# Kernel tuning notes

Measured on AMD Instinct MI355X. Metric: run time of the kernel, lower is better.

The kernel has to match this reference:

```python
import jax, jax.numpy as jnp
import numpy as np

B, S, D, H = 2, 2048, 1024, 16
HD = D // H  # head dim = 64


def setup_inputs() -> dict:
    key = jax.random.key(0)
    ks = jax.random.split(key, 5)
    scale = 0.02
    x = jax.random.normal(ks[0], (B, S, D), dtype=jnp.float32)
    Wqkv = jax.random.normal(ks[1], (D, 3 * D), dtype=jnp.float32) * scale
    bqkv = jnp.zeros((3 * D,), dtype=jnp.float32)
    Wproj = jax.random.normal(ks[2], (D, D), dtype=jnp.float32) * scale
    bproj = jnp.zeros((D,), dtype=jnp.float32)
    return {"x": x, "Wqkv": Wqkv, "bqkv": bqkv, "Wproj": Wproj, "bproj": bproj}


def reference(x, Wqkv, bqkv, Wproj, bproj):
    # fused QKV projection
    qkv = x @ Wqkv + bqkv                      # [B, S, 3D]
    q, k, v = jnp.split(qkv, 3, axis=-1)       # each [B, S, D]
    # split heads -> [B, H, S, HD]
    def heads(t):
        return t.reshape(B, S, H, HD).transpose(0, 2, 1, 3)
    q, k, v = heads(q), heads(k), heads(v)
    # scaled dot-product attention with causal mask (GPT-2 style)
    scores = jnp.einsum('bhqd,bhkd->bhqk', q, k) / jnp.sqrt(jnp.float32(HD))
    causal = jnp.tril(jnp.ones((S, S), dtype=bool))
    scores = jnp.where(causal, scores, jnp.finfo(scores.dtype).min)
    attn = jax.nn.softmax(scores, axis=-1)      # [B, H, S, S]
    out = jnp.einsum('bhqk,bhkd->bhqd', attn, v)  # [B, H, S, HD]
    out = out.transpose(0, 2, 1, 3).reshape(B, S, D)
    return out @ Wproj + bproj
```

## Files before the change

### kernel.cpp

```cpp
#include <hip/hip_runtime.h>
#include <hip/hip_bf16.h>


typedef __attribute__((ext_vector_type(8))) short short8;
typedef __attribute__((ext_vector_type(4))) float float4v;

#define S_LEN 2048
#define NHEAD 16
#define HDIM  64
#define DMODEL 1024

__device__ __forceinline__ unsigned short f2bf(float f) {
    union { float f; unsigned u; } v; v.f = f;
    unsigned r = v.u + 0x7FFF + ((v.u >> 16) & 1);
    return (unsigned short)(r >> 16);
}

__device__ __forceinline__ unsigned fbits_rn(float f) {
    union { float f; unsigned u; } v; v.f = f;
    return v.u + 0x8000u;
}

__device__ __forceinline__ void async16(const void* g, const void* l) {
    __builtin_amdgcn_global_load_lds(
        (const __attribute__((address_space(1))) unsigned int*)g,
        (__attribute__((address_space(3))) unsigned int*)l, 16, 0, 0);
}

__global__ void f32_to_bf16_v4(const float4* __restrict__ in,
                               ushort4* __restrict__ out, int n4) {
    int i = blockIdx.x * blockDim.x + threadIdx.x;
    if (i < n4) {
        float4 v = in[i];
        ushort4 o;
        o.x = f2bf(v.x); o.y = f2bf(v.y); o.z = f2bf(v.z); o.w = f2bf(v.w);
        out[i] = o;
    }
}

__global__ __launch_bounds__(256) void w_transpose_bf16(
    const float* __restrict__ Wqkv, const float* __restrict__ Wproj,
    unsigned short* __restrict__ outQ, unsigned short* __restrict__ outP) {
    __shared__ float t[64][65];
    const float* in; unsigned short* out; int N, bxl;
    if (blockIdx.x < 48) { in = Wqkv;  out = outQ; N = 3072; bxl = blockIdx.x; }
    else                 { in = Wproj; out = outP; N = 1024; bxl = blockIdx.x - 48; }
    const int K = 1024;
    const int kb = blockIdx.y * 64, nb = bxl * 64;
    const int tid = threadIdx.x;
    const int r0 = tid >> 4, c0 = (tid & 15) * 4;
#pragma unroll
    for (int g = 0; g < 4; g++) {
        float4 v = *(const float4*)(in + (size_t)(kb + g * 16 + r0) * N + nb + c0);
        t[g * 16 + r0][c0 + 0] = v.x; t[g * 16 + r0][c0 + 1] = v.y;
        t[g * 16 + r0][c0 + 2] = v.z; t[g * 16 + r0][c0 + 3] = v.w;
    }
    __syncthreads();
#pragma unroll
    for (int g = 0; g < 4; g++) {
        int n = g * 16 + r0;
        ushort4 o;
        o.x = f2bf(t[c0 + 0][n]); o.y = f2bf(t[c0 + 1][n]);
        o.z = f2bf(t[c0 + 2][n]); o.w = f2bf(t[c0 + 3][n]);
        *(ushort4*)(out + (size_t)(nb + n) * K + kb + c0) = o;
    }
}

__global__ __launch_bounds__(256) void v_pack(
    const unsigned short* __restrict__ V, unsigned short* __restrict__ Vp) {
    __shared__ unsigned short t[64 * 68];
    const int bh = blockIdx.y;
    const int c0 = blockIdx.x;
    const int s0 = c0 * 64;
    const int tid = threadIdx.x;
    const int r = tid >> 2, c4 = tid & 3;
    const size_t base = (size_t)bh * S_LEN * HDIM;
    union { uint4 v[2]; unsigned short u[16]; } d;
    const unsigned short* src = V + base + (size_t)(s0 + r) * HDIM + c4 * 16;
    d.v[0] = *(const uint4*)(src);
    d.v[1] = *(const uint4*)(src + 8);
#pragma unroll
    for (int j = 0; j < 16; j++) t[r * 68 + c4 * 16 + j] = d.u[j];
    __syncthreads();
    unsigned short* outb = Vp + ((size_t)(bh * 32 + c0)) * 4096;
#pragma unroll
    for (int pi = 0; pi < 2; pi++) {
        const int p = tid * 2 + pi;
        const int lane = p & 63, kk = (p >> 6) & 1, nt = p >> 7;
        const int q = lane >> 4, l = lane & 15;
        union { ushort4 v[2]; unsigned short u[8]; } w;
#pragma unroll
        for (int j = 0; j < 8; j++) {
            const int key = (kk * 2 + (j >> 2)) * 16 + q * 4 + (j & 3);
            w.u[j] = t[key * 68 + nt * 16 + l];
        }
        unsigned short* po = outb + ((nt * 2 + kk) * 64 + lane) * 8;
        *(ushort4*)(po) = w.v[0];
        *(ushort4*)(po + 4) = w.v[1];
    }
}

#define QSCALE 0.18033688f

__global__ __launch_bounds__(256) void gemm_qkv_kernel(
    const unsigned short* __restrict__ A,
    const unsigned short* __restrict__ Bt,
    const float* __restrict__ bias,
    unsigned short* __restrict__ out_q,
    unsigned short* __restrict__ out_kp,
    unsigned short* __restrict__ out_v,
    int M, int N, int K)
{
    __shared__ unsigned short smem[128 * 132];
    unsigned short* As = smem;
    unsigned short* Bs = smem + 8192;

    const int tid  = threadIdx.x;
    const int lane = tid & 63;
    const int wave = tid >> 6;
    const int quad = lane >> 4;
    const int l16  = lane & 15;

    const int m0 = blockIdx.y * 128;
    const int n0 = blockIdx.x * 128;
    const int wm = (wave >> 1) * 64;
    const int wn = (wave & 1) * 64;

    float4v acc[4][4];
#pragma unroll
    for (int i = 0; i < 4; i++)
#pragma unroll
        for (int j = 0; j < 4; j++) acc[i][j] = (float4v){0.f, 0.f, 0.f, 0.f};

    const int srow = lane >> 2;
    const int scol = (lane & 3) * 8;

    for (int k0 = 0; k0 < K; k0 += 64) {
        __syncthreads();
#pragma unroll
        for (int kk = 0; kk < 2; kk++)
#pragma unroll
            for (int it = 0; it < 2; it++) {
                const int rg = it * 64 + wave * 16;
                async16(A  + (size_t)(m0 + rg + srow) * K + k0 + kk * 32 + scol,
                        (const char*)(As + kk * 4096) + rg * 64);
                async16(Bt + (size_t)(n0 + rg + srow) * K + k0 + kk * 32 + scol,
                        (const char*)(Bs + kk * 4096) + rg * 64);
            }
        __syncthreads();

#pragma unroll
        for (int kk = 0; kk < 2; kk++) {
            short8 af[4], bf[4];
#pragma unroll
            for (int mt = 0; mt < 4; mt++)
                af[mt] = *(const short8*)(As + kk * 4096
                                          + (wm + mt * 16 + l16) * 32 + quad * 8);
#pragma unroll
            for (int nt = 0; nt < 4; nt++)
                bf[nt] = *(const short8*)(Bs + kk * 4096
                                          + (wn + nt * 16 + l16) * 32 + quad * 8);
#pragma unroll
            for (int mt = 0; mt < 4; mt++)
#pragma unroll
                for (int nt = 0; nt < 4; nt++)
                    acc[mt][nt] = __builtin_amdgcn_mfma_f32_16x16x32_bf16(
                        af[mt], bf[nt], acc[mt][nt], 0, 0, 0);
        }
    }

    __syncthreads();
#pragma unroll
    for (int nt = 0; nt < 4; nt++) {
        const int col = n0 + wn + nt * 16 + l16;
        const float sc = ((col >> 10) == 0) ? QSCALE : 1.0f;
        const float bia = bias[col] * sc;
        const int cold = (wn + nt * 16 + l16) >> 1;
#pragma unroll
        for (int mt = 0; mt < 4; mt++)
#pragma unroll
            for (int r = 0; r < 4; r++) {
                unsigned fb = fbits_rn(acc[mt][nt][r] * sc + bia);
                unsigned fbp = (unsigned)__shfl_xor((int)fb, 1, 64);
                unsigned pd = (l16 & 1)
                    ? __builtin_amdgcn_perm(fb, fbp, 0x07060302)
                    : __builtin_amdgcn_perm(fbp, fb, 0x07060302);
                const int rowl = wm + mt * 16 + quad * 4 + r;
                *((unsigned*)smem + rowl * 66 + cold) = pd;
            }
    }
    __syncthreads();

#pragma unroll
    for (int ps = 0; ps < 8; ps++) {
        const int row = ps * 16 + (tid >> 4);
        const int pc  = tid & 15;
        const int col0 = pc * 8;
        const int cb = n0 + (col0 >> 6) * 64;
        const int part = cb >> 10;
        const int hh = (cb & 1023) >> 6;
        const int gr = m0 + row;
        const int b = gr >> 11, s = gr & 2047;
        const size_t bhI = (size_t)(b * NHEAD + hh);
        const unsigned short* pl = smem + row * 132 + col0;
        uint2 a = *(const uint2*)(pl);
        uint2 bb = *(const uint2*)(pl + 4);
        uint4 w; w.x = a.x; w.y = a.y; w.z = bb.x; w.w = bb.y;
        unsigned short* po;
        if (part == 1) {
            const int hd = col0 & 63;
            const int h = hd >> 5, q = (hd >> 3) & 3;
            po = out_kp + ((((bhI * 32 + (s >> 6)) * 4 + ((s >> 4) & 3)) * 2 + h)
                           * 64 + q * 16 + (s & 15)) * 8;
        } else {
            unsigned short* dst = (part == 0) ? out_q : out_v;
            po = dst + (bhI * S_LEN + s) * HDIM + (col0 & 63);
        }
        *(uint4*)po = w;
    }
}

__global__ __launch_bounds__(256) void gemm_proj_kernel(
    const unsigned short* __restrict__ A,
    const unsigned short* __restrict__ Bt,
    const float* __restrict__ bias,
    float* __restrict__ out_f,
    int M, int N, int K)
{
    __shared__ unsigned short smem[12288];
    unsigned short* As = smem;
    unsigned short* Bs = smem + 4096;

    const int tid  = threadIdx.x;
    const int lane = tid & 63;
    const int wave = tid >> 6;
    const int quad = lane >> 4;
    const int l16  = lane & 15;

    const int m0 = blockIdx.y * 64;
    const int n0 = blockIdx.x * 128;
    const int wm = (wave >> 1) * 32;
    const int wn = (wave & 1) * 64;

    float4v acc[2][4];
#pragma unroll
    for (int i = 0; i < 2; i++)
#pragma unroll
        for (int j = 0; j < 4; j++) acc[i][j] = (float4v){0.f, 0.f, 0.f, 0.f};

    const int srow = lane >> 2;
    const int scol = (lane & 3) * 8;

    for (int k0 = 0; k0 < K; k0 += 64) {
        __syncthreads();
#pragma unroll
        for (int kk = 0; kk < 2; kk++) {
            async16(A + (size_t)(m0 + wave * 16 + srow) * K + k0 + kk * 32 + scol,
                    (const char*)(As + kk * 2048) + wave * 1024);
#pragma unroll
            for (int it = 0; it < 2; it++) {
                const int rg = it * 64 + wave * 16;
                async16(Bt + (size_t)(n0 + rg + srow) * K + k0 + kk * 32 + scol,
                        (const char*)(Bs + kk * 4096) + rg * 64);
            }
        }
        __syncthreads();

#pragma unroll
        for (int kk = 0; kk < 2; kk++) {
            short8 af[2], bf[4];
#pragma unroll
            for (int mt = 0; mt < 2; mt++)
                af[mt] = *(const short8*)(As + kk * 2048
                                          + (wm + mt * 16 + l16) * 32 + quad * 8);
#pragma unroll
            for (int nt = 0; nt < 4; nt++)
                bf[nt] = *(const short8*)(Bs + kk * 4096
                                          + (wn + nt * 16 + l16) * 32 + quad * 8);
#pragma unroll
            for (int mt = 0; mt < 2; mt++)
#pragma unroll
                for (int nt = 0; nt < 4; nt++)
                    acc[mt][nt] = __builtin_amdgcn_mfma_f32_16x16x32_bf16(
                        af[mt], bf[nt], acc[mt][nt], 0, 0, 0);
        }
    }

#pragma unroll
    for (int nt = 0; nt < 4; nt++) {
        const int col = n0 + wn + nt * 16 + l16;
        const float bia = bias[col];
#pragma unroll
        for (int mt = 0; mt < 2; mt++) {
            const int rowb = m0 + wm + mt * 16 + quad * 4;
#pragma unroll
            for (int r = 0; r < 4; r++)
                out_f[(size_t)(rowb + r) * N + col] = acc[mt][nt][r] + bia;
        }
    }
}

__global__ __launch_bounds__(256) void attn6_kernel(
    const unsigned short* __restrict__ Q,
    const unsigned short* __restrict__ Kp,
    const unsigned short* __restrict__ Vp,
    unsigned short* __restrict__ ctx)
{
    __shared__ unsigned short lds[2][8192];

    const int tid  = threadIdx.x;
    const int lane = tid & 63;
    const int wave = tid >> 6;
    const int quad = lane >> 4;
    const int l16  = lane & 15;

    const int bx = blockIdx.x;
    const int bh = bx & 31;
    const int qb = 31 - (bx >> 5);
    const int q0 = qb * 64 + wave * 16;
    const int nch = qb + 1;

    const size_t baseQ = (size_t)bh * S_LEN * HDIM;
    const unsigned short* kb_ = Kp + (size_t)bh * 32 * 4096;
    const unsigned short* vb_ = Vp + (size_t)bh * 32 * 4096;

    short8 qf[2];
#pragma unroll
    for (int h = 0; h < 2; h++)
        qf[h] = *(const short8*)(Q + baseQ + (size_t)(q0 + l16) * HDIM
                                 + h * 32 + quad * 8);

    float4v o[4];
#pragma unroll
    for (int nt = 0; nt < 4; nt++) o[nt] = (float4v){0.f, 0.f, 0.f, 0.f};
    float lsa[4] = {0.f, 0.f, 0.f, 0.f};

    {
        unsigned short* sb = &lds[0][0];
        async16(kb_ + tid * 8,        sb + wave * 512);
        async16(kb_ + 2048 + tid * 8, sb + 2048 + wave * 512);
        async16(vb_ + tid * 8,        sb + 4096 + wave * 512);
        async16(vb_ + 2048 + tid * 8, sb + 6144 + wave * 512);
    }

    for (int c = 0; c < nch; c++) {
        __syncthreads();
        const unsigned short* lb = &lds[c & 1][0];

        short8 kf[4][2];
#pragma unroll
        for (int kt = 0; kt < 4; kt++)
#pragma unroll
            for (int h = 0; h < 2; h++)
                kf[kt][h] = *(const short8*)(lb + ((kt * 2 + h) * 64 + lane) * 8);

        if (c + 1 < nch) {
            const unsigned short* kc = kb_ + (size_t)(c + 1) * 4096;
            const unsigned short* vc = vb_ + (size_t)(c + 1) * 4096;
            unsigned short* sb = &lds[(c + 1) & 1][0];
            async16(kc + tid * 8,        sb + wave * 512);
            async16(kc + 2048 + tid * 8, sb + 2048 + wave * 512);
            async16(vc + tid * 8,        sb + 4096 + wave * 512);
            async16(vc + 2048 + tid * 8, sb + 6144 + wave * 512);
        }

        float4v st[4];
#pragma unroll
        for (int kt = 0; kt < 4; kt++) {
            st[kt] = __builtin_amdgcn_mfma_f32_16x16x32_bf16(
                kf[kt][0], qf[0], (float4v){0.f, 0.f, 0.f, 0.f}, 0, 0, 0);
            st[kt] = __builtin_amdgcn_mfma_f32_16x16x32_bf16(
                kf[kt][1], qf[1], st[kt], 0, 0, 0);
        }

        short8 vf[4][2];
#pragma unroll
        for (int nt = 0; nt < 4; nt++)
#pragma unroll
            for (int kk = 0; kk < 2; kk++)
                vf[nt][kk] = *(const short8*)(lb + 4096
                                              + ((nt * 2 + kk) * 64 + lane) * 8);

        const bool lastc = (c == nch - 1);
        const int kb0 = c * 64;
        const int qpos = q0 + l16;
        float p[4][4];
#pragma unroll
        for (int kt = 0; kt < 4; kt++)
#pragma unroll
            for (int r = 0; r < 4; r++) {
                float x = st[kt][r];
                if (lastc) {
                    int kpos = kb0 + kt * 16 + quad * 4 + r;
                    x = (kpos <= qpos) ? x : -1e30f;
                }
                p[kt][r] = __builtin_amdgcn_exp2f(x);
                lsa[kt] += p[kt][r];
            }

        unsigned pk[4][2];
#pragma unroll
        for (int kt = 0; kt < 4; kt++)
#pragma unroll
            for (int j = 0; j < 2; j++)
                pk[kt][j] = __builtin_amdgcn_perm(
                    fbits_rn(p[kt][2 * j + 1]), fbits_rn(p[kt][2 * j]),
                    0x07060302);
        union { unsigned u[4]; short8 s; } pf[2];
#pragma unroll
        for (int kk = 0; kk < 2; kk++)
#pragma unroll
            for (int pp = 0; pp < 4; pp++)
                pf[kk].u[pp] = pk[kk * 2 + (pp >> 1)][pp & 1];

#pragma unroll
        for (int nt = 0; nt < 4; nt++) {
            o[nt] = __builtin_amdgcn_mfma_f32_16x16x32_bf16(
                pf[0].s, vf[nt][0], o[nt], 0, 0, 0);
            o[nt] = __builtin_amdgcn_mfma_f32_16x16x32_bf16(
                pf[1].s, vf[nt][1], o[nt], 0, 0, 0);
        }
    }

    float l = (lsa[0] + lsa[1]) + (lsa[2] + lsa[3]);
    l += __shfl_xor(l, 16, 64);
    l += __shfl_xor(l, 32, 64);
    const float linv = 1.f / l;
    float lr[4];
#pragma unroll
    for (int r = 0; r < 4; r++) lr[r] = __shfl(linv, quad * 4 + r, 64);

    const int b = bh >> 4, h = bh & 15;
#pragma unroll
    for (int r = 0; r < 4; r++) {
        const int s = q0 + quad * 4 + r;
        const size_t off = ((size_t)(b * S_LEN + s)) * DMODEL + h * HDIM;
#pragma unroll
        for (int nt = 0; nt < 4; nt++)
            ctx[off + nt * 16 + l16] = f2bf(o[nt][r] * lr[r]);
    }
}

extern "C" void kernel_launch(void* const* d_in, const int* in_sizes, int n_in,
                              void* d_out, int out_size, void* d_ws, size_t ws_size,
                              hipStream_t stream) {
    const float* x     = (const float*)d_in[0];
    const float* Wqkv  = (const float*)d_in[1];
    const float* bqkv  = (const float*)d_in[2];
    const float* Wproj = (const float*)d_in[3];
    const float* bproj = (const float*)d_in[4];
    float* out = (float*)d_out;

    const int M  = 2 * S_LEN;
    const int N1 = 3 * DMODEL;
    const int K  = DMODEL;

    unsigned short* x_bf    = (unsigned short*)d_ws;
    unsigned short* wqkv_t  = x_bf   + (size_t)M * K;
    unsigned short* wproj_t = wqkv_t + (size_t)K * N1;
    unsigned short* q_bf    = wproj_t + (size_t)K * DMODEL;
    unsigned short* kp_bf   = q_bf   + (size_t)M * DMODEL;
    unsigned short* v_bf    = kp_bf  + (size_t)M * DMODEL;
    unsigned short* ctx_bf  = v_bf   + (size_t)M * DMODEL;
    unsigned short* vp_bf   = x_bf;

    {
        int n4 = (M * K) / 4;
        f32_to_bf16_v4<<<n4 / 256, 256, 0, stream>>>((const float4*)x,
                                                     (ushort4*)x_bf, n4);
    }
    {
        dim3 g(64, 16);
        w_transpose_bf16<<<g, 256, 0, stream>>>(Wqkv, Wproj, wqkv_t, wproj_t);
    }

    dim3 g1(N1 / 128, M / 128);
    gemm_qkv_kernel<<<g1, 256, 0, stream>>>(x_bf, wqkv_t, bqkv,
                                            q_bf, kp_bf, v_bf, M, N1, K);

    {
        dim3 g(S_LEN / 64, 2 * NHEAD);
        v_pack<<<g, 256, 0, stream>>>(v_bf, vp_bf);
    }

    attn6_kernel<<<1024, 256, 0, stream>>>(q_bf, kp_bf, vp_bf, ctx_bf);

    dim3 g3(DMODEL / 128, M / 64);
    gemm_proj_kernel<<<g3, 256, 0, stream>>>(ctx_bf, wproj_t, bproj, out,
                                             M, DMODEL, K);
}
```

Baseline: 172.3 us.

## Double query tile per attention block to reuse K/V loads across 128 queries

Each attention block now covers 128 query rows (32 per wave, two 16-row MFMA tiles) instead of 64, so each K/V chunk staged in LDS serves twice as many queries and the grid halves to 512 blocks. Block order is interleaved so heavy and light causal blocks are mixed, and waves skip chunks that lie entirely beyond their causal range. Masking is applied per tile only where needed. In exchange each thread holds more registers for two sets of accumulators, and waves within a block have uneven work near the diagonal.

Result: slower. 184.1 us (+6.9%).

```diff
diff --git a/kernel.cpp b/kernel.cpp
--- a/kernel.cpp
+++ b/kernel.cpp
@@ -300,7 +300,7 @@
     }
 }
 
-__global__ __launch_bounds__(256) void attn6_kernel(
+__global__ __launch_bounds__(256, 2) void attn7_kernel(
     const unsigned short* __restrict__ Q,
     const unsigned short* __restrict__ Kp,
     const unsigned short* __restrict__ Vp,
@@ -316,24 +316,34 @@
 
     const int bx = blockIdx.x;
     const int bh = bx & 31;
-    const int qb = 31 - (bx >> 5);
-    const int q0 = qb * 64 + wave * 16;
-    const int nch = qb + 1;
+    const int g  = bx >> 5;
+    const int qb = (g < 8) ? (15 - g) : (g - 8);
+    const int q0w = qb * 128 + wave * 32;
+    const int nch = 2 * qb + 2;
 
     const size_t baseQ = (size_t)bh * S_LEN * HDIM;
     const unsigned short* kb_ = Kp + (size_t)bh * 32 * 4096;
     const unsigned short* vb_ = Vp + (size_t)bh * 32 * 4096;
 
-    short8 qf[2];
-#pragma unroll
-    for (int h = 0; h < 2; h++)
-        qf[h] = *(const short8*)(Q + baseQ + (size_t)(q0 + l16) * HDIM
-                                 + h * 32 + quad * 8);
-
-    float4v o[4];
-#pragma unroll
-    for (int nt = 0; nt < 4; nt++) o[nt] = (float4v){0.f, 0.f, 0.f, 0.f};
-    float lsa[4] = {0.f, 0.f, 0.f, 0.f};
+    short8 qf[2][2];
+#pragma unroll
+    for (int qt = 0; qt < 2; qt++)
+#pragma unroll
+        for (int h = 0; h < 2; h++)
+            qf[qt][h] = *(const short8*)(Q + baseQ
+                                         + (size_t)(q0w + qt * 16 + l16) * HDIM
+                                         + h * 32 + quad * 8);
+
+    float4v o[2][4];
+#pragma unroll
+    for (int qt = 0; qt < 2; qt++)
+#pragma unroll
+        for (int nt = 0; nt < 4; nt++) o[qt][nt] = (float4v){0.f, 0.f, 0.f, 0.f};
+    float lsa[2][4];
+#pragma unroll
+    for (int qt = 0; qt < 2; qt++)
+#pragma unroll
+        for (int kt = 0; kt < 4; kt++) lsa[qt][kt] = 0.f;
 
     {
         unsigned short* sb = &lds[0][0];
@@ -346,13 +356,18 @@
     for (int c = 0; c < nch; c++) {
         __syncthreads();
         const unsigned short* lb = &lds[c & 1][0];
+        const int kb0 = c * 64;
+        const bool wactive = (kb0 <= q0w + 31);
 
         short8 kf[4][2];
-#pragma unroll
-        for (int kt = 0; kt < 4; kt++)
-#pragma unroll
-            for (int h = 0; h < 2; h++)
-                kf[kt][h] = *(const short8*)(lb + ((kt * 2 + h) * 64 + lane) * 8);
+        if (wactive) {
+#pragma unroll
+            for (int kt = 0; kt < 4; kt++)
+#pragma unroll
+                for (int h = 0; h < 2; h++)
+                    kf[kt][h] = *(const short8*)(lb
+                                                 + ((kt * 2 + h) * 64 + lane) * 8);
+        }
 
         if (c + 1 < nch) {
             const unsigned short* kc = kb_ + (size_t)(c + 1) * 4096;
@@ -364,80 +379,90 @@
             async16(vc + 2048 + tid * 8, sb + 6144 + wave * 512);
         }
 
-        float4v st[4];
-#pragma unroll
-        for (int kt = 0; kt < 4; kt++) {
-            st[kt] = __builtin_amdgcn_mfma_f32_16x16x32_bf16(
-                kf[kt][0], qf[0], (float4v){0.f, 0.f, 0.f, 0.f}, 0, 0, 0);
-            st[kt] = __builtin_amdgcn_mfma_f32_16x16x32_bf16(
-                kf[kt][1], qf[1], st[kt], 0, 0, 0);
-        }
-
-        short8 vf[4][2];
-#pragma unroll
-        for (int nt = 0; nt < 4; nt++)
-#pragma unroll
-            for (int kk = 0; kk < 2; kk++)
-                vf[nt][kk] = *(const short8*)(lb + 4096
-                                              + ((nt * 2 + kk) * 64 + lane) * 8);
-
-        const bool lastc = (c == nch - 1);
-        const int kb0 = c * 64;
-        const int qpos = q0 + l16;
-        float p[4][4];
-#pragma unroll
-        for (int kt = 0; kt < 4; kt++)
-#pragma unroll
-            for (int r = 0; r < 4; r++) {
-                float x = st[kt][r];
-                if (lastc) {
-                    int kpos = kb0 + kt * 16 + quad * 4 + r;
-                    x = (kpos <= qpos) ? x : -1e30f;
+        if (wactive) {
+            float4v st[2][4];
+#pragma unroll
+            for (int qt = 0; qt < 2; qt++)
+#pragma unroll
+                for (int kt = 0; kt < 4; kt++) {
+                    st[qt][kt] = __builtin_amdgcn_mfma_f32_16x16x32_bf16(
+                        kf[kt][0], qf[qt][0], (float4v){0.f, 0.f, 0.f, 0.f},
+                        0, 0, 0);
+                    st[qt][kt] = __builtin_amdgcn_mfma_f32_16x16x32_bf16(
+                        kf[kt][1], qf[qt][1], st[qt][kt], 0, 0, 0);
                 }
-                p[kt][r] = __builtin_amdgcn_exp2f(x);
-                lsa[kt] += p[kt][r];
+
+            short8 vf[4][2];
+#pragma unroll
+            for (int nt = 0; nt < 4; nt++)
+#pragma unroll
+                for (int kk = 0; kk < 2; kk++)
+                    vf[nt][kk] = *(const short8*)(lb + 4096
+                                                  + ((nt * 2 + kk) * 64 + lane) * 8);
+
+#pragma unroll
+            for (int qt = 0; qt < 2; qt++) {
+                const int q0t = q0w + qt * 16;
+                const bool needmask = (kb0 + 63 > q0t);
+                const int qpos = q0t + l16;
+                float p[4][4];
+#pragma unroll
+                for (int kt = 0; kt < 4; kt++)
+#pragma unroll
+                    for (int r = 0; r < 4; r++) {
+                        float x = st[qt][kt][r];
+                        if (needmask) {
+                            int kpos = kb0 + kt * 16 + quad * 4 + r;
+                            x = (kpos <= qpos) ? x : -1e30f;
+                        }
+                        p[kt][r] = __builtin_amdgcn_exp2f(x);
+                        lsa[qt][kt] += p[kt][r];
+                    }
+
+                unsigned pk[4][2];
+#pragma unroll
+                for (int kt = 0; kt < 4; kt++)
+#pragma unroll
+                    for (int j = 0; j < 2; j++)
+                        pk[kt][j] = __builtin_amdgcn_perm(
+                            fbits_rn(p[kt][2 * j + 1]), fbits_rn(p[kt][2 * j]),
+                            0x07060302);
+                union { unsigned u[4]; short8 s; } pf[2];
+#pragma unroll
+                for (int kk = 0; kk < 2; kk++)
+#pragma unroll
+                    for (int pp = 0; pp < 4; pp++)
+                        pf[kk].u[pp] = pk[kk * 2 + (pp >> 1)][pp & 1];
+
+#pragma unroll
+                for (int nt = 0; nt < 4; nt++) {
+                    o[qt][nt] = __builtin_amdgcn_mfma_f32_16x16x32_bf16(
+                        pf[0].s, vf[nt][0], o[qt][nt], 0, 0, 0);
+                    o[qt][nt] = __builtin_amdgcn_mfma_f32_16x16x32_bf16(
+                        pf[1].s, vf[nt][1], o[qt][nt], 0, 0, 0);
+                }
             }
-
-        unsigned pk[4][2];
-#pragma unroll
-        for (int kt = 0; kt < 4; kt++)
-#pragma unroll
-            for (int j = 0; j < 2; j++)
-                pk[kt][j] = __builtin_amdgcn_perm(
-                    fbits_rn(p[kt][2 * j + 1]), fbits_rn(p[kt][2 * j]),
-                    0x07060302);
-        union { unsigned u[4]; short8 s; } pf[2];
-#pragma unroll
-        for (int kk = 0; kk < 2; kk++)
-#pragma unroll
-            for (int pp = 0; pp < 4; pp++)
-                pf[kk].u[pp] = pk[kk * 2 + (pp >> 1)][pp & 1];
-
-#pragma unroll
-        for (int nt = 0; nt < 4; nt++) {
-            o[nt] = __builtin_amdgcn_mfma_f32_16x16x32_bf16(
-                pf[0].s, vf[nt][0], o[nt], 0, 0, 0);
-            o[nt] = __builtin_amdgcn_mfma_f32_16x16x32_bf16(
-                pf[1].s, vf[nt][1], o[nt], 0, 0, 0);
-        }
-    }
-
-    float l = (lsa[0] + lsa[1]) + (lsa[2] + lsa[3]);
-    l += __shfl_xor(l, 16, 64);
-    l += __shfl_xor(l, 32, 64);
-    const float linv = 1.f / l;
-    float lr[4];
-#pragma unroll
-    for (int r = 0; r < 4; r++) lr[r] = __shfl(linv, quad * 4 + r, 64);
+        }
+    }
 
     const int b = bh >> 4, h = bh & 15;
 #pragma unroll
-    for (int r = 0; r < 4; r++) {
-        const int s = q0 + quad * 4 + r;
-        const size_t off = ((size_t)(b * S_LEN + s)) * DMODEL + h * HDIM;
-#pragma unroll
-        for (int nt = 0; nt < 4; nt++)
-            ctx[off + nt * 16 + l16] = f2bf(o[nt][r] * lr[r]);
+    for (int qt = 0; qt < 2; qt++) {
+        float l = (lsa[qt][0] + lsa[qt][1]) + (lsa[qt][2] + lsa[qt][3]);
+        l += __shfl_xor(l, 16, 64);
+        l += __shfl_xor(l, 32, 64);
+        const float linv = 1.f / l;
+        float lr[4];
+#pragma unroll
+        for (int r = 0; r < 4; r++) lr[r] = __shfl(linv, quad * 4 + r, 64);
+#pragma unroll
+        for (int r = 0; r < 4; r++) {
+            const int s = q0w + qt * 16 + quad * 4 + r;
+            const size_t off = ((size_t)(b * S_LEN + s)) * DMODEL + h * HDIM;
+#pragma unroll
+            for (int nt = 0; nt < 4; nt++)
+                ctx[off + nt * 16 + l16] = f2bf(o[qt][nt][r] * lr[r]);
+        }
     }
 }
 
@@ -483,7 +508,7 @@
         v_pack<<<g, 256, 0, stream>>>(v_bf, vp_bf);
     }
 
-    attn6_kernel<<<1024, 256, 0, stream>>>(q_bf, kp_bf, vp_bf, ctx_bf);
+    attn7_kernel<<<512, 256, 0, stream>>>(q_bf, kp_bf, vp_bf, ctx_bf);
 
     dim3 g3(DMODEL / 128, M / 64);
     gemm_proj_kernel<<<g3, 256, 0, stream>>>(ctx_bf, wproj_t, bproj, out,
```

## Split attention KV range in two halves and combine partials

Applied to the files above, without the earlier changes.

Each query block's causal KV chunk range is split across two workgroups (split-K style). Each writes unnormalized fp32 partial outputs and row sums to workspace, and a new combine kernel sums them, normalizes and writes bf16 context. This is meant to cut the load imbalance and tail of long causal rows, since 1024 blocks became 2048 with shorter work. In exchange it adds an extra kernel launch and about 33 MB of fp32 partial traffic through global memory. The combine without a max works only because the softmax skips max subtraction.

Result: slower. 184.1 us (+6.9%).

```diff
diff --git a/kernel.cpp b/kernel.cpp
--- a/kernel.cpp
+++ b/kernel.cpp
@@ -300,11 +300,12 @@
     }
 }
 
-__global__ __launch_bounds__(256) void attn6_kernel(
+__global__ __launch_bounds__(256) void attn9_kernel(
     const unsigned short* __restrict__ Q,
     const unsigned short* __restrict__ Kp,
     const unsigned short* __restrict__ Vp,
-    unsigned short* __restrict__ ctx)
+    float* __restrict__ op,
+    float* __restrict__ lp)
 {
     __shared__ unsigned short lds[2][8192];
 
@@ -316,9 +317,14 @@
 
     const int bx = blockIdx.x;
     const int bh = bx & 31;
-    const int qb = 31 - (bx >> 5);
+    const int r_ = 63 - (bx >> 5);
+    const int qb   = r_ >> 1;
+    const int half = r_ & 1;
+    const int n  = qb + 1;
+    const int h0 = (n + 1) >> 1;
+    const int cstart = half ? h0 : 0;
+    const int cend   = half ? n  : h0;
     const int q0 = qb * 64 + wave * 16;
-    const int nch = qb + 1;
 
     const size_t baseQ = (size_t)bh * S_LEN * HDIM;
     const unsigned short* kb_ = Kp + (size_t)bh * 32 * 4096;
@@ -335,110 +341,145 @@
     for (int nt = 0; nt < 4; nt++) o[nt] = (float4v){0.f, 0.f, 0.f, 0.f};
     float lsa[4] = {0.f, 0.f, 0.f, 0.f};
 
-    {
-        unsigned short* sb = &lds[0][0];
-        async16(kb_ + tid * 8,        sb + wave * 512);
-        async16(kb_ + 2048 + tid * 8, sb + 2048 + wave * 512);
-        async16(vb_ + tid * 8,        sb + 4096 + wave * 512);
-        async16(vb_ + 2048 + tid * 8, sb + 6144 + wave * 512);
-    }
-
-    for (int c = 0; c < nch; c++) {
-        __syncthreads();
-        const unsigned short* lb = &lds[c & 1][0];
-
-        short8 kf[4][2];
-#pragma unroll
-        for (int kt = 0; kt < 4; kt++)
-#pragma unroll
-            for (int h = 0; h < 2; h++)
-                kf[kt][h] = *(const short8*)(lb + ((kt * 2 + h) * 64 + lane) * 8);
-
-        if (c + 1 < nch) {
-            const unsigned short* kc = kb_ + (size_t)(c + 1) * 4096;
-            const unsigned short* vc = vb_ + (size_t)(c + 1) * 4096;
-            unsigned short* sb = &lds[(c + 1) & 1][0];
+    if (cstart < cend) {
+        {
+            const unsigned short* kc = kb_ + (size_t)cstart * 4096;
+            const unsigned short* vc = vb_ + (size_t)cstart * 4096;
+            unsigned short* sb = &lds[cstart & 1][0];
             async16(kc + tid * 8,        sb + wave * 512);
             async16(kc + 2048 + tid * 8, sb + 2048 + wave * 512);
             async16(vc + tid * 8,        sb + 4096 + wave * 512);
             async16(vc + 2048 + tid * 8, sb + 6144 + wave * 512);
         }
 
-        float4v st[4];
-#pragma unroll
-        for (int kt = 0; kt < 4; kt++) {
-            st[kt] = __builtin_amdgcn_mfma_f32_16x16x32_bf16(
-                kf[kt][0], qf[0], (float4v){0.f, 0.f, 0.f, 0.f}, 0, 0, 0);
-            st[kt] = __builtin_amdgcn_mfma_f32_16x16x32_bf16(
-                kf[kt][1], qf[1], st[kt], 0, 0, 0);
-        }
-
-        short8 vf[4][2];
-#pragma unroll
-        for (int nt = 0; nt < 4; nt++)
+        for (int c = cstart; c < cend; c++) {
+            __syncthreads();
+            const unsigned short* lb = &lds[c & 1][0];
+
+            short8 kf[4][2];
+#pragma unroll
+            for (int kt = 0; kt < 4; kt++)
+#pragma unroll
+                for (int h = 0; h < 2; h++)
+                    kf[kt][h] = *(const short8*)(lb
+                                                 + ((kt * 2 + h) * 64 + lane) * 8);
+
+            if (c + 1 < cend) {
+                const unsigned short* kc = kb_ + (size_t)(c + 1) * 4096;
+                const unsigned short* vc = vb_ + (size_t)(c + 1) * 4096;
+                unsigned short* sb = &lds[(c + 1) & 1][0];
+                async16(kc + tid * 8,        sb + wave * 512);
+                async16(kc + 2048 + tid * 8, sb + 2048 + wave * 512);
+                async16(vc + tid * 8,        sb + 4096 + wave * 512);
+                async16(vc + 2048 + tid * 8, sb + 6144 + wave * 512);
+            }
+
+            float4v st[4];
+#pragma unroll
+            for (int kt = 0; kt < 4; kt++) {
+                st[kt] = __builtin_amdgcn_mfma_f32_16x16x32_bf16(
+                    kf[kt][0], qf[0], (float4v){0.f, 0.f, 0.f, 0.f}, 0, 0, 0);
+                st[kt] = __builtin_amdgcn_mfma_f32_16x16x32_bf16(
+                    kf[kt][1], qf[1], st[kt], 0, 0, 0);
+            }
+
+            short8 vf[4][2];
+#pragma unroll
+            for (int nt = 0; nt < 4; nt++)
+#pragma unroll
+                for (int kk = 0; kk < 2; kk++)
+                    vf[nt][kk] = *(const short8*)(lb + 4096
+                                                  + ((nt * 2 + kk) * 64 + lane) * 8);
+
+            const int kb0 = c * 64;
+            const bool needmask = (kb0 + 63 > q0);
+            const int qpos = q0 + l16;
+            float p[4][4];
+#pragma unroll
+            for (int kt = 0; kt < 4; kt++)
+#pragma unroll
+                for (int rr = 0; rr < 4; rr++) {
+                    float x = st[kt][rr];
+                    if (needmask) {
+                        int kpos = kb0 + kt * 16 + quad * 4 + rr;
+                        x = (kpos <= qpos) ? x : -1e30f;
+                    }
+                    p[kt][rr] = __builtin_amdgcn_exp2f(x);
+                    lsa[kt] += p[kt][rr];
+                }
+
+            unsigned pk[4][2];
+#pragma unroll
+            for (int kt = 0; kt < 4; kt++)
+#pragma unroll
+                for (int j = 0; j < 2; j++)
+                    pk[kt][j] = __builtin_amdgcn_perm(
+                        fbits_rn(p[kt][2 * j + 1]), fbits_rn(p[kt][2 * j]),
+                        0x07060302);
+            union { unsigned u[4]; short8 s; } pf[2];
 #pragma unroll
             for (int kk = 0; kk < 2; kk++)
-                vf[nt][kk] = *(const short8*)(lb + 4096
-                                              + ((nt * 2 + kk) * 64 + lane) * 8);
-
-        const bool lastc = (c == nch - 1);
-        const int kb0 = c * 64;
-        const int qpos = q0 + l16;
-        float p[4][4];
-#pragma unroll
-        for (int kt = 0; kt < 4; kt++)
-#pragma unroll
-            for (int r = 0; r < 4; r++) {
-                float x = st[kt][r];
-                if (lastc) {
-                    int kpos = kb0 + kt * 16 + quad * 4 + r;
-                    x = (kpos <= qpos) ? x : -1e30f;
-                }
-                p[kt][r] = __builtin_amdgcn_exp2f(x);
-                lsa[kt] += p[kt][r];
+#pragma unroll
+                for (int pp = 0; pp < 4; pp++)
+                    pf[kk].u[pp] = pk[kk * 2 + (pp >> 1)][pp & 1];
+
+#pragma unroll
+            for (int nt = 0; nt < 4; nt++) {
+                o[nt] = __builtin_amdgcn_mfma_f32_16x16x32_bf16(
+                    pf[0].s, vf[nt][0], o[nt], 0, 0, 0);
+                o[nt] = __builtin_amdgcn_mfma_f32_16x16x32_bf16(
+                    pf[1].s, vf[nt][1], o[nt], 0, 0, 0);
             }
-
-        unsigned pk[4][2];
-#pragma unroll
-        for (int kt = 0; kt < 4; kt++)
-#pragma unroll
-            for (int j = 0; j < 2; j++)
-                pk[kt][j] = __builtin_amdgcn_perm(
-                    fbits_rn(p[kt][2 * j + 1]), fbits_rn(p[kt][2 * j]),
-                    0x07060302);
-        union { unsigned u[4]; short8 s; } pf[2];
-#pragma unroll
-        for (int kk = 0; kk < 2; kk++)
-#pragma unroll
-            for (int pp = 0; pp < 4; pp++)
-                pf[kk].u[pp] = pk[kk * 2 + (pp >> 1)][pp & 1];
-
-#pragma unroll
-        for (int nt = 0; nt < 4; nt++) {
-            o[nt] = __builtin_amdgcn_mfma_f32_16x16x32_bf16(
-                pf[0].s, vf[nt][0], o[nt], 0, 0, 0);
-            o[nt] = __builtin_amdgcn_mfma_f32_16x16x32_bf16(
-                pf[1].s, vf[nt][1], o[nt], 0, 0, 0);
         }
     }
 
     float l = (lsa[0] + lsa[1]) + (lsa[2] + lsa[3]);
     l += __shfl_xor(l, 16, 64);
     l += __shfl_xor(l, 32, 64);
-    const float linv = 1.f / l;
-    float lr[4];
-#pragma unroll
-    for (int r = 0; r < 4; r++) lr[r] = __shfl(linv, quad * 4 + r, 64);
-
+    if (lane < 16)
+        lp[((size_t)half * 32 + bh) * S_LEN + q0 + l16] = l;
+
+    float* pob = op + (((size_t)half * 32 + bh) * S_LEN) * HDIM;
+#pragma unroll
+    for (int rr = 0; rr < 4; rr++) {
+        const int s = q0 + quad * 4 + rr;
+#pragma unroll
+        for (int nt = 0; nt < 4; nt++)
+            pob[(size_t)s * HDIM + nt * 16 + l16] = o[nt][rr];
+    }
+}
+
+__global__ __launch_bounds__(256) void combine_kernel(
+    const float* __restrict__ op,
+    const float* __restrict__ lp,
+    unsigned short* __restrict__ ctx)
+{
+    const int t = blockIdx.x * 256 + threadIdx.x;
+    const int qid = t >> 3;
+    const int hd0 = (t & 7) * 8;
+    const size_t NQ = 32 * (size_t)S_LEN;
+
+    const float* p0 = op + (size_t)qid * HDIM + hd0;
+    const float* p1 = op + (NQ + qid) * HDIM + hd0;
+    float4 a0 = *(const float4*)(p0);
+    float4 a1 = *(const float4*)(p0 + 4);
+    float4 b0 = *(const float4*)(p1);
+    float4 b1 = *(const float4*)(p1 + 4);
+    const float linv = 1.f / (lp[qid] + lp[NQ + qid]);
+
+    union { ushort4 v[2]; uint4 q; } w;
+    w.v[0].x = f2bf((a0.x + b0.x) * linv);
+    w.v[0].y = f2bf((a0.y + b0.y) * linv);
+    w.v[0].z = f2bf((a0.z + b0.z) * linv);
+    w.v[0].w = f2bf((a0.w + b0.w) * linv);
+    w.v[1].x = f2bf((a1.x + b1.x) * linv);
+    w.v[1].y = f2bf((a1.y + b1.y) * linv);
+    w.v[1].z = f2bf((a1.z + b1.z) * linv);
+    w.v[1].w = f2bf((a1.w + b1.w) * linv);
+
+    const int bh = qid >> 11, s = qid & 2047;
     const int b = bh >> 4, h = bh & 15;
-#pragma unroll
-    for (int r = 0; r < 4; r++) {
-        const int s = q0 + quad * 4 + r;
-        const size_t off = ((size_t)(b * S_LEN + s)) * DMODEL + h * HDIM;
-#pragma unroll
-        for (int nt = 0; nt < 4; nt++)
-            ctx[off + nt * 16 + l16] = f2bf(o[nt][r] * lr[r]);
-    }
+    *(uint4*)(ctx + ((size_t)(b * S_LEN + s)) * DMODEL + h * HDIM + hd0) = w.q;
 }
 
 extern "C" void kernel_launch(void* const* d_in, const int* in_sizes, int n_in,
@@ -463,6 +504,8 @@
     unsigned short* v_bf    = kp_bf  + (size_t)M * DMODEL;
     unsigned short* ctx_bf  = v_bf   + (size_t)M * DMODEL;
     unsigned short* vp_bf   = x_bf;
+    float* op = (float*)(ctx_bf + (size_t)M * DMODEL);
+    float* lp = op + (size_t)2 * 32 * S_LEN * HDIM;
 
     {
         int n4 = (M * K) / 4;
@@ -483,7 +526,8 @@
         v_pack<<<g, 256, 0, stream>>>(v_bf, vp_bf);
     }
 
-    attn6_kernel<<<1024, 256, 0, stream>>>(q_bf, kp_bf, vp_bf, ctx_bf);
+    attn9_kernel<<<2048, 256, 0, stream>>>(q_bf, kp_bf, vp_bf, op, lp);
+    combine_kernel<<<2048, 256, 0, stream>>>(op, lp, ctx_bf);
 
     dim3 g3(DMODEL / 128, M / 64);
     gemm_proj_kernel<<<g3, 256, 0, stream>>>(ctx_bf, wproj_t, bproj, out,
```
